# Optimization experiments

Hardware: AMD Instinct MI355X
Metric: run time of the kernel (lower is better)

## Reference

```python
import jax, jax.numpy as jnp
import numpy as np

B, T, C = 2, 2048, 1024
NHEADS = 16
HEAD_DIM = C // NHEADS  # 64
THETA = 10000.0
SCALE_BASE = 512.0
GN_EPS = 1e-5


def setup_inputs() -> dict:
    key = jax.random.key(0)
    ks = jax.random.split(key, 4)
    s = 0.02
    return {
        "x": jax.random.normal(ks[0], (B, T, C), jnp.float32),
        "w_qkv": jax.random.normal(ks[1], (3 * C, C), jnp.float32) * s,
        "w_gated": jax.random.normal(ks[2], (C, C), jnp.float32) * s,
        "w_proj": jax.random.normal(ks[3], (C, C), jnp.float32) * s,
        "gn_weight": jnp.ones((C,), jnp.float32),
        "gn_bias": jnp.zeros((C,), jnp.float32),
    }


def _rotate_half(x):
    # pairs are adjacent/interleaved: (d r) with r=2
    x1 = x[..., 0::2]
    x2 = x[..., 1::2]
    return jnp.stack([-x2, x1], axis=-1).reshape(x.shape)


def _rope_xpos(q, k, T):
    # lucidrains rotary_embedding_torch with use_xpos=True
    d = q.shape[-1]
    half = jnp.arange(0, d, 2, dtype=jnp.float32)
    inv_freq = 1.0 / (THETA ** (half / d))
    t = jnp.arange(T, dtype=jnp.float32)
    freqs = t[:, None] * inv_freq[None, :]          # [T, d/2]
    freqs = jnp.repeat(freqs, 2, axis=-1)           # [T, d] interleaved
    scale_vec = (half + 0.4 * d) / (1.4 * d)        # [d/2]
    power = (t - T // 2) / SCALE_BASE               # [T]
    scale = scale_vec[None, :] ** power[:, None]    # [T, d/2]
    scale = jnp.repeat(scale, 2, axis=-1)           # [T, d]
    cos, sin = jnp.cos(freqs), jnp.sin(freqs)
    q = q * (cos * scale) + _rotate_half(q) * (sin * scale)
    k = k * (cos / scale) + _rotate_half(k) * (sin / scale)
    return q, k


def _decay_mask(T):
    # gamma_h = 1 - 2^(-5-h); mask[h,i,j] = gamma_h^(i-j) for i>=j else 0
    gamma = 1.0 - 2.0 ** (-5.0 - jnp.arange(NHEADS, dtype=jnp.float32))
    idx = jnp.arange(T)
    diff = idx[:, None] - idx[None, :]              # [T, T]
    causal = diff >= 0
    expn = jnp.where(causal, diff, 0).astype(jnp.float32)
    return jnp.where(causal[None], gamma[:, None, None] ** expn[None], 0.0)


def reference(x, w_qkv, w_gated, w_proj, gn_weight, gn_bias):
    Bx, Tx, Cx = x.shape
    qkv = x @ w_qkv.T                               # [B,T,3C]
    q, k, v = jnp.split(qkv, 3, axis=-1)
    def to_heads(u):
        return u.reshape(Bx, Tx, NHEADS, HEAD_DIM).transpose(0, 2, 1, 3)
    q, k, v = to_heads(q), to_heads(k), to_heads(v)  # [B,H,T,D]
    q, k = _rope_xpos(q, k, Tx)
    mask = _decay_mask(Tx)                           # [H,T,T]
    scores = jnp.einsum('bhtd,bhsd->bhts', q, k) * (HEAD_DIM ** -0.5)
    scores = scores * mask[None]
    y = jnp.einsum('bhts,bhsd->bhtd', scores, v)     # [B,H,T,D]
    y = y.transpose(0, 2, 1, 3).reshape(Bx, Tx, Cx)  # [B,T,C]
    # GroupNorm over (B, C, T) with num_groups = NHEADS: normalize each
    # group's (C/H channels x T positions) jointly.
    yt = y.transpose(0, 2, 1).reshape(Bx, NHEADS, HEAD_DIM, Tx)
    mean = yt.mean(axis=(2, 3), keepdims=True)
    var = yt.var(axis=(2, 3), keepdims=True)
    yn = (yt - mean) / jnp.sqrt(var + GN_EPS)
    yn = yn.reshape(Bx, Cx, Tx)
    yn = yn * gn_weight[None, :, None] + gn_bias[None, :, None]
    yn = yn.transpose(0, 2, 1)                       # [B,T,C]
    out = jax.nn.silu(x @ w_gated.T) * yn
    return out @ w_proj.T
```

## Files before the change

kernel.cpp:

```cpp
#include <hip/hip_runtime.h>

typedef __attribute__((ext_vector_type(8))) short bf16x8;
typedef __attribute__((ext_vector_type(4))) float f32x4;
typedef __attribute__((ext_vector_type(16))) float f32x16;
typedef __attribute__((ext_vector_type(2))) unsigned short u16x2;
typedef __attribute__((ext_vector_type(4))) unsigned short u16x4;
typedef __attribute__((ext_vector_type(2))) unsigned int u32x2;

static constexpr int kB = 2;
static constexpr int kT = 2048;
static constexpr int kC = 1024;
static constexpr int kH = 16;
static constexpr int kD = 64;
static constexpr int kNC = 16;

__device__ inline unsigned short f2bf(float f) {
    unsigned int u = __float_as_uint(f);
    u += 0x7FFFu + ((u >> 16) & 1u);
    return (unsigned short)(u >> 16);
}
__device__ inline float bf2f(unsigned short u) {
    return __uint_as_float(((unsigned int)u) << 16);
}

#define GLDS16(g, s)                                                            \
    __builtin_amdgcn_global_load_lds(                                           \
        (const __attribute__((address_space(1))) unsigned int*)(g),             \
        (__attribute__((address_space(3))) unsigned int*)(s), 16, 0, 0)

__global__ __launch_bounds__(256) void cvt_bf16(const float* __restrict__ in,
                                                unsigned short* __restrict__ out, int n) {
    int i = (blockIdx.x * 256 + threadIdx.x) * 4;
    if (i >= n) return;
    float4 v = *(const float4*)(in + i);
    u16x4 o;
    o[0] = f2bf(v.x); o[1] = f2bf(v.y); o[2] = f2bf(v.z); o[3] = f2bf(v.w);
    *(u16x4*)(out + i) = o;
}

__global__ __launch_bounds__(256) void rope_tables(float2* __restrict__ qtab,
                                                   float2* __restrict__ ktab) {
    int idx = blockIdx.x * 256 + threadIdx.x;
    if (idx >= kT * 32) return;
    int t = idx >> 5, i = idx & 31;
    float half = 2.0f * (float)i;
    float inv_freq = powf(10000.0f, -half / 64.0f);
    float fr = (float)t * inv_freq;
    float sv = (half + 0.4f * 64.0f) / (1.4f * 64.0f);
    float p = ((float)t - 1024.0f) / 512.0f;
    float scl = powf(sv, p);
    float c = cosf(fr), s = sinf(fr);
    qtab[idx] = make_float2(c * scl, s * scl);
    ktab[idx] = make_float2(c / scl, s / scl);
}

__global__ __launch_bounds__(256) void dec_tables(float* __restrict__ decq,
                                                  float* __restrict__ deck) {
    int idx = blockIdx.x * 256 + threadIdx.x;
    if (idx >= kH * 128) return;
    int h = idx >> 7, tt = idx & 127;
    float log2g = log2f(1.0f - exp2f(-5.0f - (float)h));
    decq[idx] = 0.125f * exp2f(log2g * (float)tt);
    deck[idx] = exp2f(-log2g * (float)tt);
}

__global__ __launch_bounds__(256) void gemm_qkvg(const unsigned short* __restrict__ A,
                                                 const unsigned short* __restrict__ Bm,
                                                 unsigned short* __restrict__ qb,
                                                 unsigned short* __restrict__ kbuf,
                                                 unsigned short* __restrict__ vtb,
                                                 unsigned short* __restrict__ gbuf) {
    constexpr int K = 1024;
    __shared__ __align__(16) unsigned short Al[128 * 64];
    __shared__ __align__(16) unsigned short Bl[128 * 64];
    char* ab = (char*)Al;
    char* bb = (char*)Bl;
    const int tid = threadIdx.x;
    const int l = tid & 63, w = tid >> 6;
    const int wr = w >> 1, wc = w & 1;
    const int tm = blockIdx.y * 128, tn = blockIdx.x * 128;
    const int ri = l >> 3;
    const int su = (l & 7) ^ (ri & 7);

    f32x4 zero4 = {0.0f, 0.0f, 0.0f, 0.0f};
    f32x4 acc[4][4];
#pragma unroll
    for (int m = 0; m < 4; m++)
#pragma unroll
        for (int n = 0; n < 4; n++) acc[m][n] = zero4;

    for (int kt = 0; kt < K; kt += 64) {
#pragma unroll
        for (int c = w; c < 32; c += 4) {
            if (c < 16) {
                const unsigned short* src = A + (size_t)(tm + c * 8 + ri) * K + kt + su * 8;
                GLDS16(src, ab + c * 1024);
            } else {
                int cb = c - 16;
                const unsigned short* src = Bm + (size_t)(tn + cb * 8 + ri) * K + kt + su * 8;
                GLDS16(src, bb + cb * 1024);
            }
        }
        __syncthreads();
#pragma unroll
        for (int ks = 0; ks < 2; ks++) {
            bf16x8 af[4], bfr[4];
            int kbyte = ks * 64 + (l >> 4) * 16;
#pragma unroll
            for (int m = 0; m < 4; m++) {
                int row = wr * 64 + m * 16 + (l & 15);
                af[m] = *(const bf16x8*)(ab + row * 128 + (kbyte ^ ((row & 7) << 4)));
            }
#pragma unroll
            for (int n = 0; n < 4; n++) {
                int row = wc * 64 + n * 16 + (l & 15);
                bfr[n] = *(const bf16x8*)(bb + row * 128 + (kbyte ^ ((row & 7) << 4)));
            }
#pragma unroll
            for (int m = 0; m < 4; m++)
#pragma unroll
                for (int n = 0; n < 4; n++)
                    acc[m][n] = __builtin_amdgcn_mfma_f32_16x16x32_bf16(af[m], bfr[n], acc[m][n], 0, 0, 0);
        }
        __syncthreads();
    }

    if (tn < 2048) {
        const bool isq = (tn < 1024);
        unsigned short* dst = isq ? qb : kbuf;
        const int colbase = isq ? tn : (tn - 1024);
#pragma unroll
        for (int n = 0; n < 4; n++) {
            int col = colbase + wc * 64 + n * 16 + (l & 15);
            int h = col >> 6;
            int d = col & 63;
#pragma unroll
            for (int m = 0; m < 4; m++) {
#pragma unroll
                for (int r = 0; r < 4; r++) {
                    int row = tm + wr * 64 + m * 16 + (l >> 4) * 4 + r;
                    int b = row >> 11, t = row & 2047;
                    unsigned int ub = f2bf(acc[m][n][r]);
                    unsigned int pb = (unsigned int)__shfl_xor((int)ub, 1);
                    if (!(l & 1)) {
                        unsigned int packed = (ub & 0xFFFFu) | (pb << 16);
                        *(unsigned int*)(dst + ((size_t)(b * 16 + h) * 2048 + t) * 64 + d) = packed;
                    }
                }
            }
        }
    } else if (tn < 3072) {
#pragma unroll
        for (int m = 0; m < 4; m++)
#pragma unroll
            for (int n = 0; n < 4; n++) {
                int col2 = (tn - 2048) + wc * 64 + n * 16 + (l & 15);
                int rowb = tm + wr * 64 + m * 16 + (l >> 4) * 4;
                int b = rowb >> 11, t = rowb & 2047;
                u16x4 o;
#pragma unroll
                for (int r = 0; r < 4; r++) o[r] = f2bf(acc[m][n][r]);
                *(u16x4*)(vtb + ((size_t)(b * 1024 + col2)) * 2048 + t) = o;
            }
    } else {
#pragma unroll
        for (int m = 0; m < 4; m++)
#pragma unroll
            for (int n = 0; n < 4; n++)
#pragma unroll
                for (int r = 0; r < 4; r++) {
                    int row = tm + wr * 64 + m * 16 + (l >> 4) * 4 + r;
                    int col3 = (tn - 3072) + wc * 64 + n * 16 + (l & 15);
                    float v = acc[m][n][r];
                    float sv2 = v / (1.0f + expf(-v));
                    gbuf[(size_t)row * 1024 + col3] = f2bf(sv2);
                }
    }
}

__global__ __launch_bounds__(256) void rope_qkt(unsigned short* __restrict__ qb,
                                                unsigned short* __restrict__ kbuf,
                                                unsigned short* __restrict__ ktb,
                                                const float2* __restrict__ qtab,
                                                const float2* __restrict__ ktab,
                                                const float* __restrict__ decq,
                                                const float* __restrict__ deck) {
    __shared__ unsigned short tile[64][72];
    const int bh = blockIdx.x;
    const int tt = blockIdx.y * 64;
    const int h = bh & 15;
    const int tl = threadIdx.x >> 2;
    const int du = (threadIdx.x & 3) * 16;
    const int t = tt + tl;
    const float dq = decq[h * 128 + (t & 127)];
    const float dk = deck[h * 128 + (t & 127)];

    {
        unsigned short* qrow = qb + ((size_t)bh * kT + t) * kD + du;
        bf16x8 a0 = *(const bf16x8*)(qrow);
        bf16x8 a1 = *(const bf16x8*)(qrow + 8);
        bf16x8 o0, o1;
#pragma unroll
        for (int j = 0; j < 4; ++j) {
            float2 cs = qtab[t * 32 + (du >> 1) + j];
            float x0 = bf2f((unsigned short)a0[2 * j]);
            float x1 = bf2f((unsigned short)a0[2 * j + 1]);
            o0[2 * j] = (short)f2bf((x0 * cs.x - x1 * cs.y) * dq);
            o0[2 * j + 1] = (short)f2bf((x1 * cs.x + x0 * cs.y) * dq);
            float2 cs2 = qtab[t * 32 + (du >> 1) + 4 + j];
            float y0 = bf2f((unsigned short)a1[2 * j]);
            float y1 = bf2f((unsigned short)a1[2 * j + 1]);
            o1[2 * j] = (short)f2bf((y0 * cs2.x - y1 * cs2.y) * dq);
            o1[2 * j + 1] = (short)f2bf((y1 * cs2.x + y0 * cs2.y) * dq);
        }
        *(bf16x8*)(qrow) = o0;
        *(bf16x8*)(qrow + 8) = o1;
    }
    {
        unsigned short* krow = kbuf + ((size_t)bh * kT + t) * kD + du;
        bf16x8 a0 = *(const bf16x8*)(krow);
        bf16x8 a1 = *(const bf16x8*)(krow + 8);
        bf16x8 o0, o1;
#pragma unroll
        for (int j = 0; j < 4; ++j) {
            float2 cs = ktab[t * 32 + (du >> 1) + j];
            float x0 = bf2f((unsigned short)a0[2 * j]);
            float x1 = bf2f((unsigned short)a0[2 * j + 1]);
            o0[2 * j] = (short)f2bf((x0 * cs.x - x1 * cs.y) * dk);
            o0[2 * j + 1] = (short)f2bf((x1 * cs.x + x0 * cs.y) * dk);
            float2 cs2 = ktab[t * 32 + (du >> 1) + 4 + j];
            float y0 = bf2f((unsigned short)a1[2 * j]);
            float y1 = bf2f((unsigned short)a1[2 * j + 1]);
            o1[2 * j] = (short)f2bf((y0 * cs2.x - y1 * cs2.y) * dk);
            o1[2 * j + 1] = (short)f2bf((y1 * cs2.x + y0 * cs2.y) * dk);
        }
        *(bf16x8*)(krow) = o0;
        *(bf16x8*)(krow + 8) = o1;
#pragma unroll
        for (int e = 0; e < 8; ++e) {
            tile[tl][du + e] = (unsigned short)o0[e];
            tile[tl][du + 8 + e] = (unsigned short)o1[e];
        }
    }
    __syncthreads();
    {
        int dd = threadIdx.x >> 2;
        int tb2 = (threadIdx.x & 3) * 16;
        bf16x8 o0, o1;
#pragma unroll
        for (int e = 0; e < 8; ++e) {
            o0[e] = (short)tile[tb2 + e][dd];
            o1[e] = (short)tile[tb2 + 8 + e][dd];
        }
        unsigned short* drow = ktb + ((size_t)bh * kD + dd) * kT + tt + tb2;
        *(bf16x8*)(drow) = o0;
        *(bf16x8*)(drow + 8) = o1;
    }
}

__global__ __launch_bounds__(256) void chunk_m(const unsigned short* __restrict__ ktb,
                                               const unsigned short* __restrict__ vtb,
                                               unsigned short* __restrict__ Mt) {
    __shared__ __align__(16) unsigned short Ktl[64 * 128];
    __shared__ __align__(16) unsigned short Vtl[64 * 128];
    const int tid = threadIdx.x, l = tid & 63, w = tid >> 6;
    const int bh = blockIdx.x, c = blockIdx.y, h = bh & 15;
    const int ql = l & 31, hi5 = l >> 5;
    char* kp = (char*)Ktl;
    char* vp = (char*)Vtl;
#pragma unroll
    for (int j = 0; j < 4; ++j) {
        int ch = w * 4 + j;
        int row = ch * 4 + (l >> 4);
        int u = (l & 15) ^ (row & 15);
        GLDS16(ktb + ((size_t)bh * kD + row) * kT + c * 128 + u * 8, kp + ch * 1024);
        GLDS16(vtb + ((size_t)bh * kD + row) * kT + c * 128 + u * 8, vp + ch * 1024);
    }
    __syncthreads();
    const int iw = w >> 1, jw = w & 1;
    f32x16 acc;
#pragma unroll
    for (int r = 0; r < 16; ++r) acc[r] = 0.0f;
#pragma unroll
    for (int sk = 0; sk < 8; ++sk) {
        int rowa = iw * 32 + ql;
        int rowb = jw * 32 + ql;
        bf16x8 av = *(const bf16x8*)(vp + rowa * 256 + 16 * ((2 * sk + hi5) ^ (rowa & 15)));
        bf16x8 bk = *(const bf16x8*)(kp + rowb * 256 + 16 * ((2 * sk + hi5) ^ (rowb & 15)));
        acc = __builtin_amdgcn_mfma_f32_32x32x16_bf16(av, bk, acc, 0, 0, 0);
    }
    float log2g = log2f(1.0f - exp2f(-5.0f - (float)h));
    float gC = exp2f(128.0f * log2g);
    unsigned short* mo = Mt + ((size_t)(bh * kNC + c)) * 4096;
#pragma unroll
    for (int r = 0; r < 16; ++r) {
        int row = iw * 32 + (r & 3) + 8 * (r >> 2) + 4 * hi5;
        int col = jw * 32 + ql;
        mo[row * 64 + col] = f2bf(acc[r] * gC);
    }
}

__global__ __launch_bounds__(256) void chunk_states(const unsigned short* __restrict__ Mt,
                                                    unsigned short* __restrict__ St) {
    const int bh = blockIdx.x, c = blockIdx.y, h = bh & 15;
    const int tid = threadIdx.x;
    float log2g = log2f(1.0f - exp2f(-5.0f - (float)h));
    float gC = exp2f(128.0f * log2g);
    float acc[16];
#pragma unroll
    for (int e = 0; e < 16; ++e) acc[e] = 0.0f;
    for (int j = 0; j < c; ++j) {
        const unsigned short* m = Mt + ((size_t)(bh * kNC + j)) * 4096;
#pragma unroll
        for (int k = 0; k < 4; ++k) {
            u16x4 v = *(const u16x4*)(m + (k * 256 + tid) * 4);
#pragma unroll
            for (int e = 0; e < 4; ++e) {
                float f = bf2f(v[e]);
                acc[k * 4 + e] = acc[k * 4 + e] * gC + f;
            }
        }
    }
    unsigned short* so = St + ((size_t)(bh * kNC + c)) * 4096;
#pragma unroll
    for (int k = 0; k < 4; ++k) {
        u16x4 o;
#pragma unroll
        for (int e = 0; e < 4; ++e) o[e] = f2bf(acc[k * 4 + e]);
        *(u16x4*)(so + (k * 256 + tid) * 4) = o;
    }
}

__global__ __launch_bounds__(512) void chunk_attn(const unsigned short* __restrict__ qb,
                                                  const unsigned short* __restrict__ kb,
                                                  const unsigned short* __restrict__ vtb,
                                                  const unsigned short* __restrict__ St,
                                                  unsigned short* __restrict__ yb,
                                                  float* __restrict__ part) {
    __shared__ __align__(16) unsigned short Kt[128 * 64];
    __shared__ __align__(16) unsigned short Vt[64 * 128];
    __shared__ __align__(16) unsigned short Ss[64 * 64];
    __shared__ __align__(16) unsigned short Pl[8 * 32 * 64];
    __shared__ float red[16];
    const int tid = threadIdx.x, l = tid & 63, w = tid >> 6;
    const int bh = blockIdx.x, c = blockIdx.y;
    const int qw = w >> 1, dw = w & 1;
    const int ql = l & 31, hi5 = l >> 5;
    char* kp = (char*)Kt;
    char* vp = (char*)Vt;
    char* sp = (char*)Ss;
    char* pw = (char*)Pl + w * 4096;

#pragma unroll
    for (int j = 0; j < 2; ++j) {
        int ch = w * 2 + j;
        int row = ch * 8 + (l >> 3);
        int u = (l & 7) ^ (row & 7);
        GLDS16(kb + ((size_t)bh * kT + c * 128 + row) * kD + u * 8, kp + ch * 1024);
    }
#pragma unroll
    for (int j = 0; j < 2; ++j) {
        int ch = w * 2 + j;
        int row = ch * 4 + (l >> 4);
        int u = (l & 15) ^ (row & 15);
        GLDS16(vtb + ((size_t)bh * kD + row) * kT + c * 128 + u * 8, vp + ch * 1024);
    }
    {
        int row = w * 8 + (l >> 3);
        int u = (l & 7) ^ (row & 7);
        GLDS16(St + ((size_t)(bh * kNC + c)) * 4096 + row * 64 + u * 8, sp + w * 1024);
    }
    bf16x8 aq[4];
    {
        const unsigned short* qrow = qb + ((size_t)bh * kT + c * 128 + qw * 32 + ql) * kD + hi5 * 8;
#pragma unroll
        for (int dk = 0; dk < 4; ++dk) aq[dk] = *(const bf16x8*)(qrow + dk * 16);
    }
    __syncthreads();

    f32x16 acc;
#pragma unroll
    for (int r = 0; r < 16; ++r) acc[r] = 0.0f;
    const int qidx = qw * 32 + ql;

#pragma unroll
    for (int p = 0; p < 2; ++p) {
        f32x16 sA, sB;
#pragma unroll
        for (int r = 0; r < 16; ++r) { sA[r] = 0.0f; sB[r] = 0.0f; }
#pragma unroll
        for (int dk = 0; dk < 4; ++dk) {
            int rowa = (2 * p) * 32 + ql;
            int rowb = (2 * p + 1) * 32 + ql;
            bf16x8 ka = *(const bf16x8*)(kp + rowa * 128 + 16 * ((2 * dk + hi5) ^ (rowa & 7)));
            bf16x8 kb2 = *(const bf16x8*)(kp + rowb * 128 + 16 * ((2 * dk + hi5) ^ (rowb & 7)));
            sA = __builtin_amdgcn_mfma_f32_32x32x16_bf16(ka, aq[dk], sA, 0, 0, 0);
            sB = __builtin_amdgcn_mfma_f32_32x32x16_bf16(kb2, aq[dk], sB, 0, 0, 0);
        }
#pragma unroll
        for (int sb2 = 0; sb2 < 2; ++sb2) {
            int sbase = (2 * p + sb2) * 32 + 4 * hi5;
#pragma unroll
            for (int m = 0; m < 4; ++m) {
                float v0, v1, v2, v3;
                {
                    int s0i = sbase + 8 * m;
                    float x0 = sb2 ? sB[4 * m + 0] : sA[4 * m + 0];
                    float x1 = sb2 ? sB[4 * m + 1] : sA[4 * m + 1];
                    float x2 = sb2 ? sB[4 * m + 2] : sA[4 * m + 2];
                    float x3 = sb2 ? sB[4 * m + 3] : sA[4 * m + 3];
                    v0 = (qidx >= s0i + 0) ? x0 : 0.0f;
                    v1 = (qidx >= s0i + 1) ? x1 : 0.0f;
                    v2 = (qidx >= s0i + 2) ? x2 : 0.0f;
                    v3 = (qidx >= s0i + 3) ? x3 : 0.0f;
                }
                unsigned int lo, hi;
                asm("v_cvt_pk_bf16_f32 %0, %1, %2" : "=v"(lo) : "v"(v0), "v"(v1));
                asm("v_cvt_pk_bf16_f32 %0, %1, %2" : "=v"(hi) : "v"(v2), "v"(v3));
                u32x2 pr; pr[0] = lo; pr[1] = hi;
                *(u32x2*)(pw + ql * 128 + (((sb2 * 4 + m) * 16) ^ ((ql & 7) << 4)) + hi5 * 8) = pr;
            }
        }
#pragma unroll
        for (int kki = 0; kki < 4; ++kki) {
            bf16x8 ap = *(const bf16x8*)(pw + ql * 128 + 16 * ((2 * kki + hi5) ^ (ql & 7)));
            int rowv = dw * 32 + ql;
            bf16x8 bv = *(const bf16x8*)(vp + rowv * 256 + 16 * ((2 * (4 * p + kki) + hi5) ^ (rowv & 15)));
            acc = __builtin_amdgcn_mfma_f32_32x32x16_bf16(ap, bv, acc, 0, 0, 0);
        }
    }
#pragma unroll
    for (int dk = 0; dk < 4; ++dk) {
        int rows = dw * 32 + ql;
        bf16x8 bs = *(const bf16x8*)(sp + rows * 128 + 16 * ((2 * dk + hi5) ^ (rows & 7)));
        acc = __builtin_amdgcn_mfma_f32_32x32x16_bf16(aq[dk], bs, acc, 0, 0, 0);
    }
    float s = 0.0f, s2 = 0.0f;
#pragma unroll
    for (int r = 0; r < 16; ++r) {
        int row = c * 128 + qw * 32 + (r & 3) + 8 * (r >> 2) + 4 * hi5;
        int col = dw * 32 + ql;
        unsigned short ub = f2bf(acc[r]);
        yb[((size_t)bh * kT + row) * kD + col] = ub;
        float f = bf2f(ub);
        s += f; s2 += f * f;
    }
#pragma unroll
    for (int o = 32; o > 0; o >>= 1) {
        s += __shfl_down(s, o);
        s2 += __shfl_down(s2, o);
    }
    if (l == 0) { red[w * 2] = s; red[w * 2 + 1] = s2; }
    __syncthreads();
    if (tid == 0) {
        float S = 0.0f, S2 = 0.0f;
#pragma unroll
        for (int i = 0; i < 8; i++) { S += red[2 * i]; S2 += red[2 * i + 1]; }
        part[((size_t)bh * kNC + c) * 2] = S;
        part[((size_t)bh * kNC + c) * 2 + 1] = S2;
    }
}

__global__ __launch_bounds__(64) void gn_fin(const float* __restrict__ part,
                                             float* __restrict__ stats) {
    int bh = threadIdx.x;
    if (bh >= kB * kH) return;
    float S = 0.0f, S2 = 0.0f;
#pragma unroll
    for (int i = 0; i < kNC; i++) {
        S += part[(bh * kNC + i) * 2];
        S2 += part[(bh * kNC + i) * 2 + 1];
    }
    const float inv = 1.0f / (float)(kT * kD);
    float mean = S * inv;
    float var = S2 * inv - mean * mean;
    stats[2 * bh] = mean;
    stats[2 * bh + 1] = rsqrtf(var + 1e-5f);
}

__global__ __launch_bounds__(256) void gemm_proj(const unsigned short* __restrict__ A,
                                                 const unsigned short* __restrict__ Bm,
                                                 float* __restrict__ Cf,
                                                 int N, int K) {
    __shared__ __align__(16) unsigned short Al[128 * 64];
    __shared__ __align__(16) unsigned short Bl[128 * 64];
    char* ab = (char*)Al;
    char* bb = (char*)Bl;
    const int tid = threadIdx.x;
    const int l = tid & 63, w = tid >> 6;
    const int wr = w >> 1, wc = w & 1;
    const int tm = blockIdx.y * 128, tn = blockIdx.x * 128;
    const int ri = l >> 3;
    const int su = (l & 7) ^ (ri & 7);

    f32x4 zero4 = {0.0f, 0.0f, 0.0f, 0.0f};
    f32x4 acc[4][4];
#pragma unroll
    for (int m = 0; m < 4; m++)
#pragma unroll
        for (int n = 0; n < 4; n++) acc[m][n] = zero4;

    for (int kt = 0; kt < K; kt += 64) {
#pragma unroll
        for (int c = w; c < 32; c += 4) {
            if (c < 16) {
                const unsigned short* src = A + (size_t)(tm + c * 8 + ri) * K + kt + su * 8;
                GLDS16(src, ab + c * 1024);
            } else {
                int cb = c - 16;
                const unsigned short* src = Bm + (size_t)(tn + cb * 8 + ri) * K + kt + su * 8;
                GLDS16(src, bb + cb * 1024);
            }
        }
        __syncthreads();
#pragma unroll
        for (int ks = 0; ks < 2; ks++) {
            bf16x8 af[4], bfr[4];
            int kbyte = ks * 64 + (l >> 4) * 16;
#pragma unroll
            for (int m = 0; m < 4; m++) {
                int row = wr * 64 + m * 16 + (l & 15);
                af[m] = *(const bf16x8*)(ab + row * 128 + (kbyte ^ ((row & 7) << 4)));
            }
#pragma unroll
            for (int n = 0; n < 4; n++) {
                int row = wc * 64 + n * 16 + (l & 15);
                bfr[n] = *(const bf16x8*)(bb + row * 128 + (kbyte ^ ((row & 7) << 4)));
            }
#pragma unroll
            for (int m = 0; m < 4; m++)
#pragma unroll
                for (int n = 0; n < 4; n++)
                    acc[m][n] = __builtin_amdgcn_mfma_f32_16x16x32_bf16(af[m], bfr[n], acc[m][n], 0, 0, 0);
        }
        __syncthreads();
    }
#pragma unroll
    for (int m = 0; m < 4; m++)
#pragma unroll
        for (int n = 0; n < 4; n++)
#pragma unroll
            for (int r = 0; r < 4; r++) {
                int row = tm + wr * 64 + m * 16 + (l >> 4) * 4 + r;
                int col = tn + wc * 64 + n * 16 + (l & 15);
                Cf[(size_t)row * N + col] = acc[m][n][r];
            }
}

__global__ __launch_bounds__(256) void fuse_z(const unsigned short* __restrict__ gb,
                                              const unsigned short* __restrict__ yb,
                                              const float* __restrict__ stats,
                                              const float* __restrict__ gnw,
                                              const float* __restrict__ gnb,
                                              unsigned short* __restrict__ z) {
    int idx = blockIdx.x * 256 + threadIdx.x;
    int row = idx >> 8;
    int c = (idx & 255) << 2;
    int b = row >> 11, t = row & 2047;
    int h = c >> 6, d = c & 63;
    int bh = b * kH + h;
    u16x4 gv = *(const u16x4*)(gb + (size_t)row * kC + c);
    u16x4 yv = *(const u16x4*)(yb + (((size_t)bh * kT) + t) * kD + d);
    float mean = stats[2 * bh], rstd = stats[2 * bh + 1];
    float4 wv = *(const float4*)(gnw + c);
    float4 bv = *(const float4*)(gnb + c);
    u16x4 o;
    o[0] = f2bf(bf2f(gv[0]) * ((bf2f(yv[0]) - mean) * rstd * wv.x + bv.x));
    o[1] = f2bf(bf2f(gv[1]) * ((bf2f(yv[1]) - mean) * rstd * wv.y + bv.y));
    o[2] = f2bf(bf2f(gv[2]) * ((bf2f(yv[2]) - mean) * rstd * wv.z + bv.z));
    o[3] = f2bf(bf2f(gv[3]) * ((bf2f(yv[3]) - mean) * rstd * wv.w + bv.w));
    *(u16x4*)(z + (size_t)row * kC + c) = o;
}

extern "C" void kernel_launch(void* const* d_in, const int* in_sizes, int n_in,
                              void* d_out, int out_size, void* d_ws, size_t ws_size,
                              hipStream_t stream) {
    const float* x = (const float*)d_in[0];
    const float* w_qkv = (const float*)d_in[1];
    const float* w_gated = (const float*)d_in[2];
    const float* w_proj = (const float*)d_in[3];
    const float* gnw = (const float*)d_in[4];
    const float* gnb = (const float*)d_in[5];
    float* out = (float*)d_out;
    char* ws = (char*)d_ws;

    unsigned short* xb      = (unsigned short*)(ws + 0);
    unsigned short* wqkvb   = (unsigned short*)(ws + 8388608);
    unsigned short* wgatedb = (unsigned short*)(ws + 14680064);
    unsigned short* wprojb  = (unsigned short*)(ws + 16777216);
    unsigned short* qb      = (unsigned short*)(ws + 18874368);
    unsigned short* kbuf    = (unsigned short*)(ws + 27262976);
    unsigned short* vtb     = (unsigned short*)(ws + 35651584);
    unsigned short* zb      = (unsigned short*)(ws + 44040192);
    float* part  = (float*)(ws + 44040192);
    float* stats = (float*)(ws + 52428800);
    float2* qtab = (float2*)(ws + 52429056);
    float2* ktab = (float2*)(ws + 52953344);
    float*  decq = (float*)(ws + 53477632);
    float*  deck = (float*)(ws + 53485824);
    unsigned short* Mt  = (unsigned short*)(ws + 52429056);
    unsigned short* St  = (unsigned short*)(ws + 56623360);
    unsigned short* yb  = (unsigned short*)(ws + 60817664);
    unsigned short* gbuf= (unsigned short*)(ws + 69206272);
    unsigned short* ktb = (unsigned short*)(ws + 77594880);

    cvt_bf16<<<4096, 256, 0, stream>>>(x, xb, kB * kT * kC);
    cvt_bf16<<<3072, 256, 0, stream>>>(w_qkv, wqkvb, 3 * kC * kC);
    cvt_bf16<<<1024, 256, 0, stream>>>(w_gated, wgatedb, kC * kC);
    cvt_bf16<<<1024, 256, 0, stream>>>(w_proj, wprojb, kC * kC);
    rope_tables<<<256, 256, 0, stream>>>(qtab, ktab);
    dec_tables<<<8, 256, 0, stream>>>(decq, deck);

    gemm_qkvg<<<dim3(32, 32), 256, 0, stream>>>(xb, wqkvb, qb, kbuf, vtb, gbuf);

    rope_qkt<<<dim3(kB * kH, kT / 64), 256, 0, stream>>>(qb, kbuf, ktb, qtab, ktab, decq, deck);

    chunk_m<<<dim3(kB * kH, kNC), 256, 0, stream>>>(ktb, vtb, Mt);
    chunk_states<<<dim3(kB * kH, kNC), 256, 0, stream>>>(Mt, St);
    chunk_attn<<<dim3(kB * kH, kNC), 512, 0, stream>>>(qb, kbuf, vtb, St, yb, part);

    gn_fin<<<1, 64, 0, stream>>>(part, stats);

    fuse_z<<<4096, 256, 0, stream>>>(gbuf, yb, stats, gnw, gnb, zb);

    gemm_proj<<<dim3(kC / 128, 4096 / 128), 256, 0, stream>>>(zb, wprojb, out, kC, kC);
}
```

Measured before the change: 134.3 us.

## Merge table kernels, pack gate stores, and scan chunk states sequentially

Three unrelated changes. The rope and decay table kernels are merged into one launch. The silu-gate epilogue exchanges neighbouring bf16 values with a lane shuffle so half the lanes write packed 32-bit stores. The chunk_states kernel changes from recomputing each chunk's prefix sum in its own block (quadratic reads of Mt) to one block per head doing a sequential linear scan that writes each state. This cuts redundant memory traffic and a launch, but uses fewer blocks (32) and serialises the scan.

```diff
diff --git a/kernel.cpp b/kernel.cpp
--- a/kernel.cpp
+++ b/kernel.cpp
@@ -38,30 +38,29 @@
     *(u16x4*)(out + i) = o;
 }
 
-__global__ __launch_bounds__(256) void rope_tables(float2* __restrict__ qtab,
-                                                   float2* __restrict__ ktab) {
+__global__ __launch_bounds__(256) void make_tables(float2* __restrict__ qtab,
+                                                   float2* __restrict__ ktab,
+                                                   float* __restrict__ decq,
+                                                   float* __restrict__ deck) {
     int idx = blockIdx.x * 256 + threadIdx.x;
-    if (idx >= kT * 32) return;
-    int t = idx >> 5, i = idx & 31;
-    float half = 2.0f * (float)i;
-    float inv_freq = powf(10000.0f, -half / 64.0f);
-    float fr = (float)t * inv_freq;
-    float sv = (half + 0.4f * 64.0f) / (1.4f * 64.0f);
-    float p = ((float)t - 1024.0f) / 512.0f;
-    float scl = powf(sv, p);
-    float c = cosf(fr), s = sinf(fr);
-    qtab[idx] = make_float2(c * scl, s * scl);
-    ktab[idx] = make_float2(c / scl, s / scl);
-}
-
-__global__ __launch_bounds__(256) void dec_tables(float* __restrict__ decq,
-                                                  float* __restrict__ deck) {
-    int idx = blockIdx.x * 256 + threadIdx.x;
-    if (idx >= kH * 128) return;
-    int h = idx >> 7, tt = idx & 127;
-    float log2g = log2f(1.0f - exp2f(-5.0f - (float)h));
-    decq[idx] = 0.125f * exp2f(log2g * (float)tt);
-    deck[idx] = exp2f(-log2g * (float)tt);
+    if (idx < kT * 32) {
+        int t = idx >> 5, i = idx & 31;
+        float half = 2.0f * (float)i;
+        float inv_freq = powf(10000.0f, -half / 64.0f);
+        float fr = (float)t * inv_freq;
+        float sv = (half + 0.4f * 64.0f) / (1.4f * 64.0f);
+        float p = ((float)t - 1024.0f) / 512.0f;
+        float scl = powf(sv, p);
+        float c = cosf(fr), s = sinf(fr);
+        qtab[idx] = make_float2(c * scl, s * scl);
+        ktab[idx] = make_float2(c / scl, s / scl);
+    }
+    if (idx < kH * 128) {
+        int h = idx >> 7, tt = idx & 127;
+        float log2g = log2f(1.0f - exp2f(-5.0f - (float)h));
+        decq[idx] = 0.125f * exp2f(log2g * (float)tt);
+        deck[idx] = exp2f(-log2g * (float)tt);
+    }
 }
 
 __global__ __launch_bounds__(256) void gemm_qkvg(const unsigned short* __restrict__ A,
@@ -164,17 +163,24 @@
             }
     } else {
 #pragma unroll
-        for (int m = 0; m < 4; m++)
-#pragma unroll
-            for (int n = 0; n < 4; n++)
+        for (int n = 0; n < 4; n++) {
+            int col3 = (tn - 3072) + wc * 64 + n * 16 + (l & 15);
+#pragma unroll
+            for (int m = 0; m < 4; m++) {
 #pragma unroll
                 for (int r = 0; r < 4; r++) {
                     int row = tm + wr * 64 + m * 16 + (l >> 4) * 4 + r;
-                    int col3 = (tn - 3072) + wc * 64 + n * 16 + (l & 15);
                     float v = acc[m][n][r];
                     float sv2 = v / (1.0f + expf(-v));
-                    gbuf[(size_t)row * 1024 + col3] = f2bf(sv2);
+                    unsigned int ub = f2bf(sv2);
+                    unsigned int pb = (unsigned int)__shfl_xor((int)ub, 1);
+                    if (!(l & 1)) {
+                        unsigned int packed = (ub & 0xFFFFu) | (pb << 16);
+                        *(unsigned int*)(gbuf + (size_t)row * 1024 + col3) = packed;
+                    }
                 }
+            }
+        }
     }
 }
 
@@ -302,32 +308,27 @@
 
 __global__ __launch_bounds__(256) void chunk_states(const unsigned short* __restrict__ Mt,
                                                     unsigned short* __restrict__ St) {
-    const int bh = blockIdx.x, c = blockIdx.y, h = bh & 15;
+    const int bh = blockIdx.x, h = bh & 15;
     const int tid = threadIdx.x;
     float log2g = log2f(1.0f - exp2f(-5.0f - (float)h));
     float gC = exp2f(128.0f * log2g);
-    float acc[16];
-#pragma unroll
-    for (int e = 0; e < 16; ++e) acc[e] = 0.0f;
-    for (int j = 0; j < c; ++j) {
-        const unsigned short* m = Mt + ((size_t)(bh * kNC + j)) * 4096;
+    float state[16];
+#pragma unroll
+    for (int e = 0; e < 16; ++e) state[e] = 0.0f;
+    for (int c = 0; c < kNC; ++c) {
+        unsigned short* so = St + ((size_t)(bh * kNC + c)) * 4096;
+        const unsigned short* m = Mt + ((size_t)(bh * kNC + c)) * 4096;
 #pragma unroll
         for (int k = 0; k < 4; ++k) {
+            u16x4 o;
+#pragma unroll
+            for (int e = 0; e < 4; ++e) o[e] = f2bf(state[k * 4 + e]);
+            *(u16x4*)(so + (k * 256 + tid) * 4) = o;
             u16x4 v = *(const u16x4*)(m + (k * 256 + tid) * 4);
 #pragma unroll
-            for (int e = 0; e < 4; ++e) {
-                float f = bf2f(v[e]);
-                acc[k * 4 + e] = acc[k * 4 + e] * gC + f;
-            }
-        }
-    }
-    unsigned short* so = St + ((size_t)(bh * kNC + c)) * 4096;
-#pragma unroll
-    for (int k = 0; k < 4; ++k) {
-        u16x4 o;
-#pragma unroll
-        for (int e = 0; e < 4; ++e) o[e] = f2bf(acc[k * 4 + e]);
-        *(u16x4*)(so + (k * 256 + tid) * 4) = o;
+            for (int e = 0; e < 4; ++e)
+                state[k * 4 + e] = state[k * 4 + e] * gC + bf2f(v[e]);
+        }
     }
 }
 
@@ -608,15 +609,14 @@
     cvt_bf16<<<3072, 256, 0, stream>>>(w_qkv, wqkvb, 3 * kC * kC);
     cvt_bf16<<<1024, 256, 0, stream>>>(w_gated, wgatedb, kC * kC);
     cvt_bf16<<<1024, 256, 0, stream>>>(w_proj, wprojb, kC * kC);
-    rope_tables<<<256, 256, 0, stream>>>(qtab, ktab);
-    dec_tables<<<8, 256, 0, stream>>>(decq, deck);
+    make_tables<<<256, 256, 0, stream>>>(qtab, ktab, decq, deck);
 
     gemm_qkvg<<<dim3(32, 32), 256, 0, stream>>>(xb, wqkvb, qb, kbuf, vtb, gbuf);
 
     rope_qkt<<<dim3(kB * kH, kT / 64), 256, 0, stream>>>(qb, kbuf, ktb, qtab, ktab, decq, deck);
 
     chunk_m<<<dim3(kB * kH, kNC), 256, 0, stream>>>(ktb, vtb, Mt);
-    chunk_states<<<dim3(kB * kH, kNC), 256, 0, stream>>>(Mt, St);
+    chunk_states<<<kB * kH, 256, 0, stream>>>(Mt, St);
     chunk_attn<<<dim3(kB * kH, kNC), 512, 0, stream>>>(qb, kbuf, vtb, St, yb, part);
 
     gn_fin<<<1, 64, 0, stream>>>(part, stats);
```

Result: slower. 139.0 us (+3.5%).
